# Performance work log

Hardware: AMD Instinct MI355X
Metric: run time of the kernel (lower is better)

The kernel has to match this reference:

```python
import jax, jax.numpy as jnp
import numpy as np

FEATURE_DIM = 2048
CROP_PE_DIM = 96
FULL = FEATURE_DIM + CROP_PE_DIM  # 2144
H1 = 1024
H2 = 512
NEG_SLOPE = 0.01


def leaky(x):
    return jnp.where(x >= 0, x, NEG_SLOPE * x)


def setup_inputs() -> dict:
    key = jax.random.key(0)
    ks = jax.random.split(key, 8)
    B, T = 512, 32
    features = jax.random.normal(ks[0], (B, T, FULL), dtype=jnp.float32)

    def lin(k, fan_in, fan_out):
        kw, kb = jax.random.split(k)
        bound = 1.0 / np.sqrt(fan_in)
        W = jax.random.uniform(kw, (fan_in, fan_out), minval=-bound, maxval=bound, dtype=jnp.float32)
        b = jax.random.uniform(kb, (fan_out,), minval=-bound, maxval=bound, dtype=jnp.float32)
        return W, b

    We, be = lin(ks[1], 2 * FULL, H1)
    W1a, b1a = lin(ks[2], H1, H1)
    W1b, b1b = lin(ks[3], H1, H2)
    W2a, b2a = lin(ks[4], H2, H2)
    W2b, b2b = lin(ks[5], H2, H2)
    Wd, bd = lin(ks[6], H2, 3)
    return {
        "features": features,
        "We": We, "be": be,
        "W1a": W1a, "b1a": b1a, "W1b": W1b, "b1b": b1b,
        "W2a": W2a, "b2a": b2a, "W2b": W2b, "b2b": b2b,
        "Wd": Wd, "bd": bd,
    }


def reference(features, We, be, W1a, b1a, W1b, b1b, W2a, b2a, W2b, b2b, Wd, bd):
    B, T, D = features.shape
    # Vectorized version of the double Python loop: pair each token with token 0.
    anchor = jnp.broadcast_to(features[:, :1, :], (B, T, D))  # features[i][0]
    features_full = jnp.concatenate((features, anchor), axis=-1).reshape(B * T, 2 * D)
    e_f = features_full @ We + be
    h = leaky(leaky(e_f) @ W1a + b1a)
    h = h @ W1b + b1b  # block1 output
    h2 = leaky(leaky(h) @ W2a + b2a) @ W2b + b2b  # block2
    h = h + h2
    translations = leaky(h) @ Wd + bd  # (B*T, 3)
    bias = jnp.array([[0.0, 0.0, 1.0]], dtype=translations.dtype)
    return translations + bias
```

## Files before the change

### kernel.cpp

```cpp
#include <hip/hip_runtime.h>
#include <hip/hip_bf16.h>
#include <stdint.h>

typedef __attribute__((ext_vector_type(4))) float f32x4;
typedef __attribute__((ext_vector_type(8))) short bf16x8;
typedef __attribute__((ext_vector_type(4))) short bf16x4;

#define BK 64

__device__ inline void gload_lds16(const void* g, void* l) {
    __builtin_amdgcn_global_load_lds(
        (const __attribute__((address_space(1))) void*)g,
        (__attribute__((address_space(3))) void*)l, 16, 0, 0);
}

__device__ inline void wg_barrier() {
    asm volatile("s_barrier" ::: "memory");
}
#define SCHED0 __builtin_amdgcn_sched_barrier(0)
#define VMW(n) asm volatile("s_waitcnt vmcnt(" #n ")" ::: "memory")

__device__ inline int xcd_swizzle(int orig, int nwg) {
    int q = nwg >> 3, r = nwg & 7;
    int xcd = orig & 7, idx = orig >> 3;
    int base = (xcd < r) ? xcd * (q + 1) : r * (q + 1) + (xcd - r) * q;
    return base + idx;
}

__device__ inline float b2f(short s) {
    union { float f; unsigned u; } x; x.u = ((unsigned)(unsigned short)s) << 16; return x.f;
}
__device__ inline short f2bs(float f) {
    __hip_bfloat16 h = __float2bfloat16(f);
    short s; __builtin_memcpy(&s, &h, 2); return s;
}

__device__ inline void wt_tile(const float* __restrict__ W, __hip_bfloat16* __restrict__ WT,
                               int K, int N, int KP, int tid, int bid) {
    __shared__ float tile[32][33];
    const int ntn = N >> 5;
    const int tk = bid / ntn, tn = bid - tk * ntn;
    const int k0 = tk * 32, n0 = tn * 32;
    const int c = tid & 31, r8 = tid >> 5;
    #pragma unroll
    for (int p = 0; p < 4; p++) {
        int k = k0 + r8 + p * 8;
        tile[r8 + p * 8][c] = (k < K) ? W[(size_t)k * N + n0 + c] : 0.f;
    }
    __syncthreads();
    #pragma unroll
    for (int p = 0; p < 4; p++) {
        int n = n0 + r8 + p * 8;
        WT[(size_t)n * KP + k0 + c] = __float2bfloat16(tile[c][r8 + p * 8]);
    }
}

#define NWTB 6400
#define NFTB 2048

__global__ __launch_bounds__(256)
void prepass(const float* __restrict__ feat, __hip_bfloat16* __restrict__ featbf,
             const float* __restrict__ We, __hip_bfloat16* __restrict__ WeTt,
             __hip_bfloat16* __restrict__ WeTb,
             const float* __restrict__ W1a, __hip_bfloat16* __restrict__ W1aT,
             const float* __restrict__ W1b, __hip_bfloat16* __restrict__ W1bT,
             const float* __restrict__ W2a, __hip_bfloat16* __restrict__ W2aT,
             const float* __restrict__ W2b, __hip_bfloat16* __restrict__ W2bT)
{
    const int bid = blockIdx.x;
    const int tid = threadIdx.x;
    if (bid < NWTB) {
        int b = bid;
        if      (b < 2176) wt_tile(We,                WeTt, 2144, 1024, 2176, tid, b);
        else if (b < 4352) wt_tile(We + 2144 * 1024,  WeTb, 2144, 1024, 2176, tid, b - 2176);
        else if (b < 5376) wt_tile(W1a, W1aT, 1024, 1024, 1024, tid, b - 4352);
        else if (b < 5888) wt_tile(W1b, W1bT, 1024,  512, 1024, tid, b - 5376);
        else if (b < 6144) wt_tile(W2a, W2aT,  512,  512,  512, tid, b - 5888);
        else               wt_tile(W2b, W2bT,  512,  512,  512, tid, b - 6144);
        return;
    }
    for (int r = bid - NWTB; r < 16384; r += NFTB) {
        const float* src = feat + (size_t)r * 2144;
        __hip_bfloat16* dst = featbf + (size_t)r * 2176;
        #pragma unroll
        for (int k = 0; k < 2; ++k) {
            const int i4 = tid + k * 256;
            f32x4 x = *(const f32x4*)(src + i4 * 4);
            bf16x4 o = { f2bs(x.x), f2bs(x.y), f2bs(x.z), f2bs(x.w) };
            *(bf16x4*)(dst + i4 * 4) = o;
        }
        const int i4 = 512 + tid;
        if (i4 < 536) {
            f32x4 x = *(const f32x4*)(src + i4 * 4);
            bf16x4 o = { f2bs(x.x), f2bs(x.y), f2bs(x.z), f2bs(x.w) };
            *(bf16x4*)(dst + i4 * 4) = o;
        } else if (i4 < 544) {
            bf16x4 z = { f2bs(0.f), f2bs(0.f), f2bs(0.f), f2bs(0.f) };
            *(bf16x4*)(dst + i4 * 4) = z;
        }
    }
}

template<int BN_, int RES_MODE, int OUTK>
__global__ __launch_bounds__(512, 2)
void gemmk(const __hip_bfloat16* __restrict__ A, int lda,
           const __hip_bfloat16* __restrict__ Bt,
           const float* __restrict__ bias,
           const __hip_bfloat16* __restrict__ resb,
           const float* __restrict__ resf,
           __hip_bfloat16* __restrict__ outb,
           __hip_bfloat16* __restrict__ outb2,
           float* __restrict__ outf,
           int M, int N, int K, int gx)
{
    constexpr int NF  = BN_ / 64;
    constexpr int REL = NF * 16;
    __shared__ __hip_bfloat16 lds[2][(256 + BN_) * BK];

    const int nwg  = gridDim.x;
    const int wgid = xcd_swizzle(blockIdx.x, nwg);
    const int by   = wgid / gx;
    const int bx   = wgid - by * gx;

    const int t    = threadIdx.x;
    const int lane = t & 63;
    const int wv   = t >> 6;
    const int wr   = wv >> 2;
    const int wc   = wv & 3;

    const int row0 = by * 256;
    const int col0 = bx * BN_;

    const int NT = K / BK;
    const int split = blockIdx.y;
    const int kb = (split * NT) / gridDim.y;
    const int ke = ((split + 1) * NT) / gridDim.y;
    float* outfs = outf;
    if (OUTK == 0 && gridDim.y > 1) outfs = outf + (size_t)split * M * N;

    const int srow = t >> 3;
    const int sc8  = (t & 7) * 8;
    const int scol = sc8 ^ ((srow & 7) << 3);
    const int sdst = sc8;

    f32x4 acc[8][NF];
    #pragma unroll
    for (int i = 0; i < 8; i++)
        #pragma unroll
        for (int j = 0; j < NF; j++)
            acc[i][j] = f32x4{0.f, 0.f, 0.f, 0.f};

    const int lrow = lane & 15;
    const int lk   = (lane >> 4) * 8;
    const int rxor = (lrow & 7) << 3;

    auto stA = [&](int buf, int k0, int b) {
        gload_lds16(A + (size_t)(row0 + b * 64 + srow) * lda + k0 + scol,
                    &lds[buf][(b * 64 + srow) * BK + sdst]);
    };
    auto stB = [&](int buf, int k0, int b) {
        gload_lds16(Bt + (size_t)(col0 + b * 64 + srow) * K + k0 + scol,
                    &lds[buf][(256 + b * 64 + srow) * BK + sdst]);
    };

    bf16x8 af[4][2];
    auto rdA = [&](int buf, int ih) {
        #pragma unroll
        for (int i = 0; i < 4; ++i)
            #pragma unroll
            for (int h = 0; h < 2; ++h)
                af[i][h] = *(const bf16x8*)
                    &lds[buf][(wr * 128 + (ih * 4 + i) * 16 + lrow) * BK + ((h * 32 + lk) ^ rxor)];
    };
    bf16x8 bgl[2][2], bgh[2][2];
    auto rdB2 = [&](int buf, int jb, bf16x8 (&bg)[2][2]) {
        #pragma unroll
        for (int j = 0; j < 2; ++j)
            #pragma unroll
            for (int h = 0; h < 2; ++h)
                bg[j][h] = *(const bf16x8*)
                    &lds[buf][(256 + wc * REL + (jb + j) * 16 + lrow) * BK + ((h * 32 + lk) ^ rxor)];
    };

#define MFMA_Q(BG, IB, JB)                                                    \
    do {                                                                      \
        __builtin_amdgcn_s_setprio(1);                                        \
        _Pragma("unroll") for (int h_ = 0; h_ < 2; ++h_)                      \
        _Pragma("unroll") for (int i_ = 0; i_ < 4; ++i_)                      \
        _Pragma("unroll") for (int j_ = 0; j_ < 2; ++j_)                      \
            acc[(IB) + i_][(JB) + j_] = __builtin_amdgcn_mfma_f32_16x16x32_bf16( \
                af[i_][h_], BG[j_][h_], acc[(IB) + i_][(JB) + j_], 0, 0, 0);  \
        __builtin_amdgcn_s_setprio(0);                                        \
    } while (0)

    {
        const int k0 = kb * BK, k1 = (kb + 1) * BK;
        if constexpr (NF == 4) {
            stA(0, k0, 0); stA(0, k0, 2); stA(0, k0, 1); stA(0, k0, 3);
            stB(0, k0, 0); stB(0, k0, 1); stB(0, k0, 2); stB(0, k0, 3);
            stA(1, k1, 0); stA(1, k1, 2); stA(1, k1, 1); stA(1, k1, 3);
        } else {
            stA(0, k0, 0); stA(0, k0, 2); stB(0, k0, 0); stB(0, k0, 1);
            stA(0, k0, 1); stA(0, k0, 3);
            stA(1, k1, 0); stA(1, k1, 2); stB(1, k1, 0); stB(1, k1, 1);
        }
    }

    int cur = 0;
    for (int kt = kb; kt < ke; ++kt) {
        const bool pf1 = (kt + 1 < ke), pf2 = (kt + 2 < ke);
        const int nk1 = (kt + 1) * BK, nk2 = (kt + 2) * BK;
        const int nxt = cur ^ 1;
        if constexpr (NF == 4) {
            if (kt == ke - 1) VMW(0); else VMW(4);
            wg_barrier();
            rdA(cur, 0); rdB2(cur, 0, bgl);
            if (pf1) { stB(nxt, nk1, 0); stB(nxt, nk1, 1); }
            SCHED0;
            MFMA_Q(bgl, 0, 0);
            wg_barrier();
            rdB2(cur, 2, bgh);
            if (pf1) { stB(nxt, nk1, 2); stB(nxt, nk1, 3); }
            SCHED0;
            MFMA_Q(bgh, 0, 2);
            wg_barrier();
            rdA(cur, 1);
            if (pf2) { stA(cur, nk2, 0); stA(cur, nk2, 2); }
            SCHED0;
            MFMA_Q(bgl, 4, 0);
            wg_barrier();
            if (pf2) { stA(cur, nk2, 1); stA(cur, nk2, 3); }
            SCHED0;
            MFMA_Q(bgh, 4, 2);
        } else {
            if (kt == ke - 1) VMW(2); else VMW(6);
            wg_barrier();
            rdA(cur, 0); rdB2(cur, 0, bgl);
            if (pf1) { stA(nxt, nk1, 1); stA(nxt, nk1, 3); }
            SCHED0;
            MFMA_Q(bgl, 0, 0);
            if (kt == ke - 1) VMW(0); else VMW(6);
            wg_barrier();
            rdA(cur, 1);
            if (pf2) { stA(cur, nk2, 0); stA(cur, nk2, 2); stB(cur, nk2, 0); stB(cur, nk2, 1); }
            SCHED0;
            MFMA_Q(bgl, 4, 0);
        }
        cur ^= 1;
    }
#undef MFMA_Q

    if constexpr (OUTK == 0) {
        #pragma unroll
        for (int j = 0; j < NF; j++) {
            const int col = col0 + wc * REL + j * 16 + lrow;
            #pragma unroll
            for (int i = 0; i < 8; i++) {
                const int rbase = row0 + wr * 128 + i * 16 + (lane >> 4) * 4;
                #pragma unroll
                for (int r = 0; r < 4; r++)
                    outfs[(size_t)(rbase + r) * N + col] = acc[i][j][r];
            }
        }
    } else {
        wg_barrier();
        __hip_bfloat16* eb = &lds[0][0] + wv * (128 * REL);
        #pragma unroll
        for (int i = 0; i < 8; i++)
            #pragma unroll
            for (int j = 0; j < NF; j++)
                #pragma unroll
                for (int r = 0; r < 4; r++)
                    eb[(i * 16 + (lane >> 4) * 4 + r) * REL + j * 16 + lrow] =
                        __float2bfloat16(acc[i][j][r]);
        constexpr int LPR = REL / 8;
        constexpr int RPI = 64 / LPR;
        constexpr int NIT = 128 / RPI;
        const int lrr = lane / LPR;
        const int lcc = (lane % LPR) * 8;
        const int col = col0 + wc * REL + lcc;
        float bvv[8];
        if (bias) {
            float4 b0 = *(const float4*)&bias[col];
            float4 b1 = *(const float4*)&bias[col + 4];
            bvv[0] = b0.x; bvv[1] = b0.y; bvv[2] = b0.z; bvv[3] = b0.w;
            bvv[4] = b1.x; bvv[5] = b1.y; bvv[6] = b1.z; bvv[7] = b1.w;
        } else {
            #pragma unroll
            for (int e = 0; e < 8; e++) bvv[e] = 0.f;
        }
        #pragma unroll
        for (int it = 0; it < NIT; it++) {
            const int rl  = it * RPI + lrr;
            const int row = row0 + wr * 128 + rl;
            bf16x8 v8 = *(bf16x8*)&eb[rl * REL + lcc];
            float vv[8];
            #pragma unroll
            for (int e = 0; e < 8; e++) vv[e] = b2f(v8[e]) + bvv[e];
            if constexpr (RES_MODE == 1) {
                bf16x8 r8 = *(const bf16x8*)&resb[(size_t)row * N + col];
                #pragma unroll
                for (int e = 0; e < 8; e++) vv[e] += b2f(r8[e]);
            }
            if constexpr (RES_MODE == 2) {
                const float* rp = &resf[(size_t)(row >> 5) * N + col];
                float4 r0 = *(const float4*)rp;
                float4 r1 = *(const float4*)(rp + 4);
                vv[0] += r0.x; vv[1] += r0.y; vv[2] += r0.z; vv[3] += r0.w;
                vv[4] += r1.x; vv[5] += r1.y; vv[6] += r1.z; vv[7] += r1.w;
            }
            bf16x8 o1, o2;
            #pragma unroll
            for (int e = 0; e < 8; e++) {
                float lv = vv[e] >= 0.f ? vv[e] : 0.01f * vv[e];
                if constexpr (OUTK == 1) o1[e] = f2bs(lv);
                if constexpr (OUTK == 2) o1[e] = f2bs(vv[e]);
                if constexpr (OUTK == 3) { o1[e] = f2bs(lv); o2[e] = f2bs(vv[e]); }
            }
            *(bf16x8*)&outb[(size_t)row * N + col] = o1;
            if constexpr (OUTK == 3)
                *(bf16x8*)&outb2[(size_t)row * N + col] = o2;
        }
    }
}

__global__ __launch_bounds__(256)
void anchor_reduce(const float* __restrict__ part, const float* __restrict__ be,
                   float* __restrict__ out) {
    int i = blockIdx.x * 256 + threadIdx.x;
    if (i >= 512 * 1024) return;
    const int S = 512 * 1024;
    int col = i & 1023;
    float s = be[col];
    #pragma unroll
    for (int p = 0; p < 8; p++) s += part[i + p * S];
    out[i] = s;
}

__global__ __launch_bounds__(256)
void final_head(const __hip_bfloat16* __restrict__ h, const float* __restrict__ Wd,
                const float* __restrict__ bd, float* __restrict__ out)
{
    int row  = blockIdx.x * 4 + (threadIdx.x >> 6);
    int lane = threadIdx.x & 63;
    const __hip_bfloat16* hr = h + (size_t)row * 512;
    bf16x8 v8 = *(const bf16x8*)&hr[lane * 8];
    float s0 = 0.f, s1 = 0.f, s2 = 0.f;
    #pragma unroll
    for (int e = 0; e < 8; e++) {
        float v = b2f(v8[e]);
        v = v >= 0.f ? v : 0.01f * v;
        int k = lane * 8 + e;
        s0 += v * Wd[k * 3 + 0];
        s1 += v * Wd[k * 3 + 1];
        s2 += v * Wd[k * 3 + 2];
    }
    #pragma unroll
    for (int off = 32; off > 0; off >>= 1) {
        s0 += __shfl_down(s0, off);
        s1 += __shfl_down(s1, off);
        s2 += __shfl_down(s2, off);
    }
    if (lane == 0) {
        out[row * 3 + 0] = s0 + bd[0];
        out[row * 3 + 1] = s1 + bd[1];
        out[row * 3 + 2] = s2 + bd[2] + 1.0f;
    }
}

extern "C" void kernel_launch(void* const* d_in, const int* in_sizes, int n_in,
                              void* d_out, int out_size, void* d_ws, size_t ws_size,
                              hipStream_t stream)
{
    const float* features = (const float*)d_in[0];
    const float* We  = (const float*)d_in[1];
    const float* be  = (const float*)d_in[2];
    const float* W1a = (const float*)d_in[3];
    const float* b1a = (const float*)d_in[4];
    const float* W1b = (const float*)d_in[5];
    const float* b1b = (const float*)d_in[6];
    const float* W2a = (const float*)d_in[7];
    const float* b2a = (const float*)d_in[8];
    const float* W2b = (const float*)d_in[9];
    const float* b2b = (const float*)d_in[10];
    const float* Wd  = (const float*)d_in[11];
    const float* bd  = (const float*)d_in[12];
    float* out = (float*)d_out;

    char* ws = (char*)d_ws;
    size_t off = 0;
    auto alloc = [&](size_t bytes) -> char* {
        char* p = ws + off;
        off += (bytes + 255) & ~(size_t)255;
        return p;
    };
    __hip_bfloat16* featbf = (__hip_bfloat16*)alloc(16384ull * 2176 * 2);
    __hip_bfloat16* WeTt   = (__hip_bfloat16*)alloc(1024ull * 2176 * 2);
    __hip_bfloat16* WeTb   = (__hip_bfloat16*)alloc(1024ull * 2176 * 2);
    __hip_bfloat16* W1aT   = (__hip_bfloat16*)alloc(1024ull * 1024 * 2);
    __hip_bfloat16* W1bT   = (__hip_bfloat16*)alloc(512ull * 1024 * 2);
    __hip_bfloat16* W2aT   = (__hip_bfloat16*)alloc(512ull * 512 * 2);
    __hip_bfloat16* W2bT   = (__hip_bfloat16*)alloc(512ull * 512 * 2);
    float* eanchor_part    = (float*)alloc(8ull * 512 * 1024 * 4);
    float* eanchor         = (float*)alloc(512ull * 1024 * 4);
    char* bufA             = alloc(16384ull * 1024 * 2);
    char* bufB             = alloc(16384ull * 1024 * 2);
    __hip_bfloat16* h1b    = (__hip_bfloat16*)alloc(16384ull * 512 * 2);

    __hip_bfloat16* act1   = (__hip_bfloat16*)bufA;
    __hip_bfloat16* act2   = (__hip_bfloat16*)bufB;
    __hip_bfloat16* act3   = (__hip_bfloat16*)bufA;
    __hip_bfloat16* act4   = (__hip_bfloat16*)bufB;
    __hip_bfloat16* hsum_b = (__hip_bfloat16*)bufA;

    prepass<<<NWTB + NFTB, 256, 0, stream>>>(
        features, featbf, We, WeTt, WeTb, W1a, W1aT, W1b, W1bT, W2a, W2aT, W2b, W2bT);

    gemmk<256, 0, 0><<<dim3(8, 8), 512, 0, stream>>>(
        featbf, 32 * 2176, WeTb, nullptr, nullptr, nullptr,
        nullptr, nullptr, eanchor_part, 512, 1024, 2176, 4);
    anchor_reduce<<<2048, 256, 0, stream>>>(eanchor_part, be, eanchor);

    gemmk<256, 2, 1><<<dim3(256), 512, 0, stream>>>(
        featbf, 2176, WeTt, nullptr, nullptr, eanchor,
        act1, nullptr, nullptr, 16384, 1024, 2176, 4);

    gemmk<256, 0, 1><<<dim3(256), 512, 0, stream>>>(
        act1, 1024, W1aT, b1a, nullptr, nullptr,
        act2, nullptr, nullptr, 16384, 1024, 1024, 4);

    gemmk<128, 0, 3><<<dim3(256), 512, 0, stream>>>(
        act2, 1024, W1bT, b1b, nullptr, nullptr,
        act3, h1b, nullptr, 16384, 512, 1024, 4);

    gemmk<128, 0, 1><<<dim3(256), 512, 0, stream>>>(
        act3, 512, W2aT, b2a, nullptr, nullptr,
        act4, nullptr, nullptr, 16384, 512, 512, 4);

    gemmk<128, 1, 2><<<dim3(256), 512, 0, stream>>>(
        act4, 512, W2bT, b2b, h1b, nullptr,
        hsum_b, nullptr, nullptr, 16384, 512, 512, 4);

    final_head<<<4096, 256, 0, stream>>>(hsum_b, Wd, bd, out);
}
```

Baseline: 233.0 us.

## Fuse fp32-to-bf16 feature conversion into the first GEMM's A-tile loader

Drops the prepass that converted the 16384x2144 fp32 features to a padded bf16 buffer. A new gemmf kernel reads fp32 features directly through registers, converts them to bf16, and writes them to LDS, with zero-fill for the K padding. It is used for both the anchor GEMM and the main embedding GEMM. This saves a full write and re-read of the bf16 feature copy. In exchange the A operand no longer uses async global-to-LDS loads, the fp32 A loads are twice the bytes, and the pipeline adds extra barriers and register pressure.

```diff
diff --git a/kernel.cpp b/kernel.cpp
--- a/kernel.cpp
+++ b/kernel.cpp
@@ -19,6 +19,7 @@
 }
 #define SCHED0 __builtin_amdgcn_sched_barrier(0)
 #define VMW(n) asm volatile("s_waitcnt vmcnt(" #n ")" ::: "memory")
+#define LGKM0  asm volatile("s_waitcnt lgkmcnt(0)" ::: "memory")
 
 __device__ inline int xcd_swizzle(int orig, int nwg) {
     int q = nwg >> 3, r = nwg & 7;
@@ -56,47 +57,222 @@
 }
 
 #define NWTB 6400
-#define NFTB 2048
 
 __global__ __launch_bounds__(256)
-void prepass(const float* __restrict__ feat, __hip_bfloat16* __restrict__ featbf,
-             const float* __restrict__ We, __hip_bfloat16* __restrict__ WeTt,
+void prepass(const float* __restrict__ We, __hip_bfloat16* __restrict__ WeTt,
              __hip_bfloat16* __restrict__ WeTb,
              const float* __restrict__ W1a, __hip_bfloat16* __restrict__ W1aT,
              const float* __restrict__ W1b, __hip_bfloat16* __restrict__ W1bT,
              const float* __restrict__ W2a, __hip_bfloat16* __restrict__ W2aT,
              const float* __restrict__ W2b, __hip_bfloat16* __restrict__ W2bT)
 {
-    const int bid = blockIdx.x;
+    const int b = blockIdx.x;
     const int tid = threadIdx.x;
-    if (bid < NWTB) {
-        int b = bid;
-        if      (b < 2176) wt_tile(We,                WeTt, 2144, 1024, 2176, tid, b);
-        else if (b < 4352) wt_tile(We + 2144 * 1024,  WeTb, 2144, 1024, 2176, tid, b - 2176);
-        else if (b < 5376) wt_tile(W1a, W1aT, 1024, 1024, 1024, tid, b - 4352);
-        else if (b < 5888) wt_tile(W1b, W1bT, 1024,  512, 1024, tid, b - 5376);
-        else if (b < 6144) wt_tile(W2a, W2aT,  512,  512,  512, tid, b - 5888);
-        else               wt_tile(W2b, W2bT,  512,  512,  512, tid, b - 6144);
-        return;
-    }
-    for (int r = bid - NWTB; r < 16384; r += NFTB) {
-        const float* src = feat + (size_t)r * 2144;
-        __hip_bfloat16* dst = featbf + (size_t)r * 2176;
-        #pragma unroll
-        for (int k = 0; k < 2; ++k) {
-            const int i4 = tid + k * 256;
-            f32x4 x = *(const f32x4*)(src + i4 * 4);
-            bf16x4 o = { f2bs(x.x), f2bs(x.y), f2bs(x.z), f2bs(x.w) };
-            *(bf16x4*)(dst + i4 * 4) = o;
-        }
-        const int i4 = 512 + tid;
-        if (i4 < 536) {
-            f32x4 x = *(const f32x4*)(src + i4 * 4);
-            bf16x4 o = { f2bs(x.x), f2bs(x.y), f2bs(x.z), f2bs(x.w) };
-            *(bf16x4*)(dst + i4 * 4) = o;
-        } else if (i4 < 544) {
-            bf16x4 z = { f2bs(0.f), f2bs(0.f), f2bs(0.f), f2bs(0.f) };
-            *(bf16x4*)(dst + i4 * 4) = z;
+    if      (b < 2176) wt_tile(We,                WeTt, 2144, 1024, 2176, tid, b);
+    else if (b < 4352) wt_tile(We + 2144 * 1024,  WeTb, 2144, 1024, 2176, tid, b - 2176);
+    else if (b < 5376) wt_tile(W1a, W1aT, 1024, 1024, 1024, tid, b - 4352);
+    else if (b < 5888) wt_tile(W1b, W1bT, 1024,  512, 1024, tid, b - 5376);
+    else if (b < 6144) wt_tile(W2a, W2aT,  512,  512,  512, tid, b - 5888);
+    else               wt_tile(W2b, W2bT,  512,  512,  512, tid, b - 6144);
+}
+
+template<int RES_MODE, int OUTK>
+__global__ __launch_bounds__(512, 2)
+void gemmf(const float* __restrict__ Af, int lda, int amult, int Kreal,
+           const __hip_bfloat16* __restrict__ Bt,
+           const float* __restrict__ resf,
+           __hip_bfloat16* __restrict__ outb,
+           float* __restrict__ outf,
+           int M, int N, int K, int gx)
+{
+    constexpr int REL = 64;
+    __shared__ __hip_bfloat16 lds[2][(256 + 256) * BK];
+
+    const int nwg  = gridDim.x;
+    const int wgid = xcd_swizzle(blockIdx.x, nwg);
+    const int by   = wgid / gx;
+    const int bx   = wgid - by * gx;
+
+    const int t    = threadIdx.x;
+    const int lane = t & 63;
+    const int wv   = t >> 6;
+    const int wr   = wv >> 2;
+    const int wc   = wv & 3;
+
+    const int row0 = by * 256;
+    const int col0 = bx * 256;
+
+    const int NT = K / BK;
+    const int split = blockIdx.y;
+    const int kb = (split * NT) / gridDim.y;
+    const int ke = ((split + 1) * NT) / gridDim.y;
+    float* outfs = outf;
+    if (OUTK == 0 && gridDim.y > 1) outfs = outf + (size_t)split * M * N;
+
+    const int srow = t >> 3;
+    const int sc8  = (t & 7) * 8;
+    const int sswz = (srow & 7) << 3;
+    const int scol = sc8 ^ sswz;
+    const int sdst = sc8;
+
+    f32x4 acc[8][4];
+    #pragma unroll
+    for (int i = 0; i < 8; i++)
+        #pragma unroll
+        for (int j = 0; j < 4; j++)
+            acc[i][j] = f32x4{0.f, 0.f, 0.f, 0.f};
+
+    const int lrow = lane & 15;
+    const int lk   = (lane >> 4) * 8;
+    const int rxor = (lrow & 7) << 3;
+
+    f32x4 ar[8];
+
+    auto ldA = [&](int k0) {
+        const int gc = k0 + sc8;
+        const bool v = gc < Kreal;
+        const int go = v ? gc : 0;
+        #pragma unroll
+        for (int b = 0; b < 4; ++b) {
+            const float* p = Af + (size_t)(row0 + b * 64 + srow) * (size_t)amult * lda + go;
+            f32x4 x0 = *(const f32x4*)p;
+            f32x4 x1 = *(const f32x4*)(p + 4);
+            ar[b * 2]     = v ? x0 : f32x4{0.f, 0.f, 0.f, 0.f};
+            ar[b * 2 + 1] = v ? x1 : f32x4{0.f, 0.f, 0.f, 0.f};
+        }
+    };
+    auto wrA = [&](int buf) {
+        #pragma unroll
+        for (int b = 0; b < 4; ++b) {
+            f32x4 x0 = ar[b * 2], x1 = ar[b * 2 + 1];
+            bf16x8 w;
+            w[0] = f2bs(x0[0]); w[1] = f2bs(x0[1]); w[2] = f2bs(x0[2]); w[3] = f2bs(x0[3]);
+            w[4] = f2bs(x1[0]); w[5] = f2bs(x1[1]); w[6] = f2bs(x1[2]); w[7] = f2bs(x1[3]);
+            *(bf16x8*)&lds[buf][(b * 64 + srow) * BK + (sc8 ^ sswz)] = w;
+        }
+    };
+    auto stB = [&](int buf, int k0, int b) {
+        gload_lds16(Bt + (size_t)(col0 + b * 64 + srow) * K + k0 + scol,
+                    &lds[buf][(256 + b * 64 + srow) * BK + sdst]);
+    };
+
+    bf16x8 af[4][2];
+    auto rdA = [&](int buf, int ih) {
+        #pragma unroll
+        for (int i = 0; i < 4; ++i)
+            #pragma unroll
+            for (int h = 0; h < 2; ++h)
+                af[i][h] = *(const bf16x8*)
+                    &lds[buf][(wr * 128 + (ih * 4 + i) * 16 + lrow) * BK + ((h * 32 + lk) ^ rxor)];
+    };
+    bf16x8 bgl[2][2], bgh[2][2];
+    auto rdB2 = [&](int buf, int jb, bf16x8 (&bg)[2][2]) {
+        #pragma unroll
+        for (int j = 0; j < 2; ++j)
+            #pragma unroll
+            for (int h = 0; h < 2; ++h)
+                bg[j][h] = *(const bf16x8*)
+                    &lds[buf][(256 + wc * REL + (jb + j) * 16 + lrow) * BK + ((h * 32 + lk) ^ rxor)];
+    };
+
+#define MFMA_Q(BG, IB, JB)                                                    \
+    do {                                                                      \
+        __builtin_amdgcn_s_setprio(1);                                        \
+        _Pragma("unroll") for (int h_ = 0; h_ < 2; ++h_)                      \
+        _Pragma("unroll") for (int i_ = 0; i_ < 4; ++i_)                      \
+        _Pragma("unroll") for (int j_ = 0; j_ < 2; ++j_)                      \
+            acc[(IB) + i_][(JB) + j_] = __builtin_amdgcn_mfma_f32_16x16x32_bf16( \
+                af[i_][h_], BG[j_][h_], acc[(IB) + i_][(JB) + j_], 0, 0, 0);  \
+        __builtin_amdgcn_s_setprio(0);                                        \
+    } while (0)
+
+    ldA(kb * BK);
+    stB(0, kb * BK, 0); stB(0, kb * BK, 1);
+    stB(0, kb * BK, 2); stB(0, kb * BK, 3);
+    VMW(4);
+    wrA(0);
+    ldA((kb + 1) * BK);
+    VMW(8);
+    LGKM0;
+    wg_barrier();
+
+    int cur = 0;
+    for (int kt = kb; kt < ke; ++kt) {
+        const bool pf1 = (kt + 1 < ke), pf2 = (kt + 2 < ke);
+        const int nk1 = (kt + 1) * BK, nk2 = (kt + 2) * BK;
+        const int nxt = cur ^ 1;
+        rdA(cur, 0); rdB2(cur, 0, bgl);
+        if (pf1) { stB(nxt, nk1, 0); stB(nxt, nk1, 1); }
+        SCHED0;
+        MFMA_Q(bgl, 0, 0);
+        wg_barrier();
+        rdB2(cur, 2, bgh);
+        if (pf1) { stB(nxt, nk1, 2); stB(nxt, nk1, 3); }
+        SCHED0;
+        MFMA_Q(bgh, 0, 2);
+        wg_barrier();
+        rdA(cur, 1);
+        if (pf1) { VMW(4); wrA(nxt); }
+        if (pf2) ldA(nk2);
+        SCHED0;
+        MFMA_Q(bgl, 4, 0);
+        wg_barrier();
+        MFMA_Q(bgh, 4, 2);
+        if (kt >= ke - 2) VMW(0); else VMW(8);
+        LGKM0;
+        wg_barrier();
+        cur ^= 1;
+    }
+#undef MFMA_Q
+
+    if constexpr (OUTK == 0) {
+        #pragma unroll
+        for (int j = 0; j < 4; j++) {
+            const int col = col0 + wc * REL + j * 16 + lrow;
+            #pragma unroll
+            for (int i = 0; i < 8; i++) {
+                const int rbase = row0 + wr * 128 + i * 16 + (lane >> 4) * 4;
+                #pragma unroll
+                for (int r = 0; r < 4; r++)
+                    outfs[(size_t)(rbase + r) * N + col] = acc[i][j][r];
+            }
+        }
+    } else {
+        wg_barrier();
+        __hip_bfloat16* eb = &lds[0][0] + wv * (128 * REL);
+        #pragma unroll
+        for (int i = 0; i < 8; i++)
+            #pragma unroll
+            for (int j = 0; j < 4; j++)
+                #pragma unroll
+                for (int r = 0; r < 4; r++)
+                    eb[(i * 16 + (lane >> 4) * 4 + r) * REL + j * 16 + lrow] =
+                        __float2bfloat16(acc[i][j][r]);
+        const int lrr = lane / 8;
+        const int lcc = (lane % 8) * 8;
+        const int col = col0 + wc * REL + lcc;
+        #pragma unroll
+        for (int it = 0; it < 16; it++) {
+            const int rl  = it * 8 + lrr;
+            const int row = row0 + wr * 128 + rl;
+            bf16x8 v8 = *(bf16x8*)&eb[rl * REL + lcc];
+            float vv[8];
+            #pragma unroll
+            for (int e = 0; e < 8; e++) vv[e] = b2f(v8[e]);
+            if constexpr (RES_MODE == 2) {
+                const float* rp = &resf[(size_t)(row >> 5) * N + col];
+                float4 r0 = *(const float4*)rp;
+                float4 r1 = *(const float4*)(rp + 4);
+                vv[0] += r0.x; vv[1] += r0.y; vv[2] += r0.z; vv[3] += r0.w;
+                vv[4] += r1.x; vv[5] += r1.y; vv[6] += r1.z; vv[7] += r1.w;
+            }
+            bf16x8 o1;
+            #pragma unroll
+            for (int e = 0; e < 8; e++) {
+                float lv = vv[e] >= 0.f ? vv[e] : 0.01f * vv[e];
+                o1[e] = f2bs(lv);
+            }
+            *(bf16x8*)&outb[(size_t)row * N + col] = o1;
         }
     }
 }
@@ -107,10 +283,8 @@
            const __hip_bfloat16* __restrict__ Bt,
            const float* __restrict__ bias,
            const __hip_bfloat16* __restrict__ resb,
-           const float* __restrict__ resf,
            __hip_bfloat16* __restrict__ outb,
            __hip_bfloat16* __restrict__ outb2,
-           float* __restrict__ outf,
            int M, int N, int K, int gx)
 {
     constexpr int NF  = BN_ / 64;
@@ -131,12 +305,7 @@
     const int row0 = by * 256;
     const int col0 = bx * BN_;
 
-    const int NT = K / BK;
-    const int split = blockIdx.y;
-    const int kb = (split * NT) / gridDim.y;
-    const int ke = ((split + 1) * NT) / gridDim.y;
-    float* outfs = outf;
-    if (OUTK == 0 && gridDim.y > 1) outfs = outf + (size_t)split * M * N;
+    const int kb = 0, ke = K / BK;
 
     const int srow = t >> 3;
     const int sc8  = (t & 7) * 8;
@@ -250,77 +419,56 @@
     }
 #undef MFMA_Q
 
-    if constexpr (OUTK == 0) {
-        #pragma unroll
-        for (int j = 0; j < NF; j++) {
-            const int col = col0 + wc * REL + j * 16 + lrow;
-            #pragma unroll
-            for (int i = 0; i < 8; i++) {
-                const int rbase = row0 + wr * 128 + i * 16 + (lane >> 4) * 4;
-                #pragma unroll
-                for (int r = 0; r < 4; r++)
-                    outfs[(size_t)(rbase + r) * N + col] = acc[i][j][r];
-            }
-        }
+    wg_barrier();
+    __hip_bfloat16* eb = &lds[0][0] + wv * (128 * REL);
+    #pragma unroll
+    for (int i = 0; i < 8; i++)
+        #pragma unroll
+        for (int j = 0; j < NF; j++)
+            #pragma unroll
+            for (int r = 0; r < 4; r++)
+                eb[(i * 16 + (lane >> 4) * 4 + r) * REL + j * 16 + lrow] =
+                    __float2bfloat16(acc[i][j][r]);
+    constexpr int LPR = REL / 8;
+    constexpr int RPI = 64 / LPR;
+    constexpr int NIT = 128 / RPI;
+    const int lrr = lane / LPR;
+    const int lcc = (lane % LPR) * 8;
+    const int col = col0 + wc * REL + lcc;
+    float bvv[8];
+    if (bias) {
+        float4 b0 = *(const float4*)&bias[col];
+        float4 b1 = *(const float4*)&bias[col + 4];
+        bvv[0] = b0.x; bvv[1] = b0.y; bvv[2] = b0.z; bvv[3] = b0.w;
+        bvv[4] = b1.x; bvv[5] = b1.y; bvv[6] = b1.z; bvv[7] = b1.w;
     } else {
-        wg_barrier();
-        __hip_bfloat16* eb = &lds[0][0] + wv * (128 * REL);
-        #pragma unroll
-        for (int i = 0; i < 8; i++)
-            #pragma unroll
-            for (int j = 0; j < NF; j++)
-                #pragma unroll
-                for (int r = 0; r < 4; r++)
-                    eb[(i * 16 + (lane >> 4) * 4 + r) * REL + j * 16 + lrow] =
-                        __float2bfloat16(acc[i][j][r]);
-        constexpr int LPR = REL / 8;
-        constexpr int RPI = 64 / LPR;
-        constexpr int NIT = 128 / RPI;
-        const int lrr = lane / LPR;
-        const int lcc = (lane % LPR) * 8;
-        const int col = col0 + wc * REL + lcc;
-        float bvv[8];
-        if (bias) {
-            float4 b0 = *(const float4*)&bias[col];
-            float4 b1 = *(const float4*)&bias[col + 4];
-            bvv[0] = b0.x; bvv[1] = b0.y; bvv[2] = b0.z; bvv[3] = b0.w;
-            bvv[4] = b1.x; bvv[5] = b1.y; bvv[6] = b1.z; bvv[7] = b1.w;
-        } else {
-            #pragma unroll
-            for (int e = 0; e < 8; e++) bvv[e] = 0.f;
-        }
-        #pragma unroll
-        for (int it = 0; it < NIT; it++) {
-            const int rl  = it * RPI + lrr;
-            const int row = row0 + wr * 128 + rl;
-            bf16x8 v8 = *(bf16x8*)&eb[rl * REL + lcc];
-            float vv[8];
-            #pragma unroll
-            for (int e = 0; e < 8; e++) vv[e] = b2f(v8[e]) + bvv[e];
-            if constexpr (RES_MODE == 1) {
-                bf16x8 r8 = *(const bf16x8*)&resb[(size_t)row * N + col];
-                #pragma unroll
-                for (int e = 0; e < 8; e++) vv[e] += b2f(r8[e]);
-            }
-            if constexpr (RES_MODE == 2) {
-                const float* rp = &resf[(size_t)(row >> 5) * N + col];
-                float4 r0 = *(const float4*)rp;
-                float4 r1 = *(const float4*)(rp + 4);
-                vv[0] += r0.x; vv[1] += r0.y; vv[2] += r0.z; vv[3] += r0.w;
-                vv[4] += r1.x; vv[5] += r1.y; vv[6] += r1.z; vv[7] += r1.w;
-            }
-            bf16x8 o1, o2;
-            #pragma unroll
-            for (int e = 0; e < 8; e++) {
-                float lv = vv[e] >= 0.f ? vv[e] : 0.01f * vv[e];
-                if constexpr (OUTK == 1) o1[e] = f2bs(lv);
-                if constexpr (OUTK == 2) o1[e] = f2bs(vv[e]);
-                if constexpr (OUTK == 3) { o1[e] = f2bs(lv); o2[e] = f2bs(vv[e]); }
-            }
-            *(bf16x8*)&outb[(size_t)row * N + col] = o1;
-            if constexpr (OUTK == 3)
-                *(bf16x8*)&outb2[(size_t)row * N + col] = o2;
-        }
+        #pragma unroll
+        for (int e = 0; e < 8; e++) bvv[e] = 0.f;
+    }
+    #pragma unroll
+    for (int it = 0; it < NIT; it++) {
+        const int rl  = it * RPI + lrr;
+        const int row = row0 + wr * 128 + rl;
+        bf16x8 v8 = *(bf16x8*)&eb[rl * REL + lcc];
+        float vv[8];
+        #pragma unroll
+        for (int e = 0; e < 8; e++) vv[e] = b2f(v8[e]) + bvv[e];
+        if constexpr (RES_MODE == 1) {
+            bf16x8 r8 = *(const bf16x8*)&resb[(size_t)row * N + col];
+            #pragma unroll
+            for (int e = 0; e < 8; e++) vv[e] += b2f(r8[e]);
+        }
+        bf16x8 o1, o2;
+        #pragma unroll
+        for (int e = 0; e < 8; e++) {
+            float lv = vv[e] >= 0.f ? vv[e] : 0.01f * vv[e];
+            if constexpr (OUTK == 1) o1[e] = f2bs(lv);
+            if constexpr (OUTK == 2) o1[e] = f2bs(vv[e]);
+            if constexpr (OUTK == 3) { o1[e] = f2bs(lv); o2[e] = f2bs(vv[e]); }
+        }
+        *(bf16x8*)&outb[(size_t)row * N + col] = o1;
+        if constexpr (OUTK == 3)
+            *(bf16x8*)&outb2[(size_t)row * N + col] = o2;
     }
 }
 
@@ -394,7 +542,6 @@
         off += (bytes + 255) & ~(size_t)255;
         return p;
     };
-    __hip_bfloat16* featbf = (__hip_bfloat16*)alloc(16384ull * 2176 * 2);
     __hip_bfloat16* WeTt   = (__hip_bfloat16*)alloc(1024ull * 2176 * 2);
     __hip_bfloat16* WeTb   = (__hip_bfloat16*)alloc(1024ull * 2176 * 2);
     __hip_bfloat16* W1aT   = (__hip_bfloat16*)alloc(1024ull * 1024 * 2);
@@ -413,33 +560,29 @@
     __hip_bfloat16* act4   = (__hip_bfloat16*)bufB;
     __hip_bfloat16* hsum_b = (__hip_bfloat16*)bufA;
 
-    prepass<<<NWTB + NFTB, 256, 0, stream>>>(
-        features, featbf, We, WeTt, WeTb, W1a, W1aT, W1b, W1bT, W2a, W2aT, W2b, W2bT);
-
-    gemmk<256, 0, 0><<<dim3(8, 8), 512, 0, stream>>>(
-        featbf, 32 * 2176, WeTb, nullptr, nullptr, nullptr,
-        nullptr, nullptr, eanchor_part, 512, 1024, 2176, 4);
+    prepass<<<NWTB, 256, 0, stream>>>(
+        We, WeTt, WeTb, W1a, W1aT, W1b, W1bT, W2a, W2aT, W2b, W2bT);
+
+    gemmf<0, 0><<<dim3(8, 8), 512, 0, stream>>>(
+        features, 2144, 32, 2144, WeTb, nullptr,
+        nullptr, eanchor_part, 512, 1024, 2176, 4);
     anchor_reduce<<<2048, 256, 0, stream>>>(eanchor_part, be, eanchor);
 
-    gemmk<256, 2, 1><<<dim3(256), 512, 0, stream>>>(
-        featbf, 2176, WeTt, nullptr, nullptr, eanchor,
-        act1, nullptr, nullptr, 16384, 1024, 2176, 4);
+    gemmf<2, 1><<<dim3(256), 512, 0, stream>>>(
+        features, 2144, 1, 2144, WeTt, eanchor,
+        act1, nullptr, 16384, 1024, 2176, 4);
 
     gemmk<256, 0, 1><<<dim3(256), 512, 0, stream>>>(
-        act1, 1024, W1aT, b1a, nullptr, nullptr,
-        act2, nullptr, nullptr, 16384, 1024, 1024, 4);
+        act1, 1024, W1aT, b1a, nullptr, act2, nullptr, 16384, 1024, 1024, 4);
 
     gemmk<128, 0, 3><<<dim3(256), 512, 0, stream>>>(
-        act2, 1024, W1bT, b1b, nullptr, nullptr,
-        act3, h1b, nullptr, 16384, 512, 1024, 4);
+        act2, 1024, W1bT, b1b, nullptr, act3, h1b, 16384, 512, 1024, 4);
 
     gemmk<128, 0, 1><<<dim3(256), 512, 0, stream>>>(
-        act3, 512, W2aT, b2a, nullptr, nullptr,
-        act4, nullptr, nullptr, 16384, 512, 512, 4);
+        act3, 512, W2aT, b2a, nullptr, act4, nullptr, 16384, 512, 512, 4);
 
     gemmk<128, 1, 2><<<dim3(256), 512, 0, stream>>>(
-        act4, 512, W2bT, b2b, h1b, nullptr,
-        hsum_b, nullptr, nullptr, 16384, 512, 512, 4);
+        act4, 512, W2bT, b2b, h1b, hsum_b, nullptr, 16384, 512, 512, 4);
 
     final_head<<<4096, 256, 0, stream>>>(hsum_b, Wd, bd, out);
 }
```

New measurement: 260.7 us. 1.12x slower.
